# Kernel tuning notes

Measured on AMD Instinct MI355X. Metric: run time of the kernel, lower is better.

The kernel has to match this reference:

```python
import jax, jax.numpy as jnp
import numpy as np

# dims: T time steps, B batch, F clinical features, H GRU hidden, NH heads, DFF ffn dim, AH single-attn hidden
T, B, F, H, NH, DFF, AH = 128, 256, 76, 64, 4, 256, 8


def setup_inputs() -> dict:
    key = jax.random.key(0)
    ks = jax.random.split(key, 32)
    s = 0.1
    def u(k, shape):
        return jax.random.uniform(k, shape, jnp.float32, -s, s)
    return {
        "x": jax.random.normal(ks[0], (T, B, F), jnp.float32),
        # per-feature GRU(1, H) weight stacks (torch gate order: r, z, n)
        "gru_w_ih": u(ks[1], (F, 3 * H)),          # input dim is 1 -> squeezed
        "gru_w_hh": u(ks[2], (F, 3 * H, H)),
        "gru_b_ih": jnp.zeros((F, 3 * H), jnp.float32),
        "gru_b_hh": jnp.zeros((F, 3 * H), jnp.float32),
        # per-feature SingleAttention('new', time_aware) params
        "att_Wt": u(ks[3], (F, H, AH)),
        "att_Wx": u(ks[4], (F, H, AH)),
        "att_rate": jnp.full((F,), 0.8, jnp.float32),
        # multi-head self-attention over the feature axis
        "mha_wq": u(ks[5], (H, H)), "mha_bq": jnp.zeros((H,), jnp.float32),
        "mha_wk": u(ks[6], (H, H)), "mha_bk": jnp.zeros((H,), jnp.float32),
        "mha_wv": u(ks[7], (H, H)), "mha_bv": jnp.zeros((H,), jnp.float32),
        "mha_wo": u(ks[8], (H, H)), "mha_bo": jnp.zeros((H,), jnp.float32),
        # position-wise feed forward
        "ffn_w1": u(ks[9], (H, DFF)), "ffn_b1": jnp.zeros((DFF,), jnp.float32),
        "ffn_w2": u(ks[10], (DFF, H)), "ffn_b2": jnp.zeros((H,), jnp.float32),
        # FinalAttentionQKV ('mul')
        "fa_wq": u(ks[11], (H, H)), "fa_bq": jnp.zeros((H,), jnp.float32),
        "fa_wk": u(ks[12], (H, H)), "fa_bk": jnp.zeros((H,), jnp.float32),
        "fa_wv": u(ks[13], (H, H)), "fa_bv": jnp.zeros((H,), jnp.float32),
        # output head
        "out0_w": u(ks[14], (H, H)), "out0_b": jnp.zeros((H,), jnp.float32),
        "out1_w": u(ks[15], (H, 1)), "out1_b": jnp.zeros((1,), jnp.float32),
    }


def reference(x, gru_w_ih, gru_w_hh, gru_b_ih, gru_b_hh,
              att_Wt, att_Wx, att_rate,
              mha_wq, mha_bq, mha_wk, mha_bk, mha_wv, mha_bv, mha_wo, mha_bo,
              ffn_w1, ffn_b1, ffn_w2, ffn_b2,
              fa_wq, fa_bq, fa_wk, fa_bk, fa_wv, fa_bv,
              out0_w, out0_b, out1_w, out1_b):
    # x: (T, B, F); torch permutes to (B, T, F)
    Ts, Bsz, Fd = x.shape
    Hd = gru_w_hh.shape[-1]
    dk = Hd // NH

    # ---- all F GRU(1,H) channels fused into one scan (vectorized over F) ----
    xs = jnp.transpose(x, (0, 2, 1))  # (T, F, B)

    def step(h, x_t):  # h: (F,B,H), x_t: (F,B)
        gx = x_t[:, :, None] * gru_w_ih[:, None, :] + gru_b_ih[:, None, :]      # (F,B,3H)
        gh = jnp.einsum('fbh,fgh->fbg', h, gru_w_hh) + gru_b_hh[:, None, :]     # (F,B,3H)
        rx, zx, nx = jnp.split(gx, 3, axis=-1)
        rh, zh, nh = jnp.split(gh, 3, axis=-1)
        r = jax.nn.sigmoid(rx + rh)
        z = jax.nn.sigmoid(zx + zh)
        n = jnp.tanh(nx + r * nh)
        h_new = (1.0 - z) * n + z * h
        return h_new, h_new

    h0 = jnp.zeros((Fd, Bsz, Hd), x.dtype)
    _, hs = jax.lax.scan(step, h0, xs)        # (T, F, B, H)
    hs = jnp.transpose(hs, (1, 2, 0, 3))       # (F, B, T, H)

    # ---- per-feature SingleAttention, type='new', time-aware ----
    q = jnp.einsum('fbh,fha->fba', hs[:, :, -1, :], att_Wt)   # (F,B,AH)
    k = jnp.einsum('fbth,fha->fbta', hs, att_Wx)              # (F,B,T,AH)
    dp = jnp.einsum('fba,fbta->fbt', q, k)                    # (F,B,T)
    sig = jax.nn.sigmoid(dp)
    decay = jnp.arange(Ts, 0, -1, dtype=x.dtype)              # T..1 (time_decays + 1)
    denom = jax.nn.sigmoid(att_rate)[:, None, None] * (jnp.log(2.72 + (1.0 - sig)) * decay)
    e = jax.nn.relu(sig / denom)
    a = jax.nn.softmax(e, axis=-1)
    emb = jnp.einsum('fbt,fbth->bfh', a, hs)                  # (B, F, H)

    def lin(t, w, b):
        return t @ w + b

    # ---- multi-head self-attention over the F axis + residual ----
    # NOTE: original lambda ignores its (layernormed) argument, so LN is dead code.
    def heads(t):
        return t.reshape(Bsz, Fd, NH, dk).transpose(0, 2, 1, 3)
    qh = heads(lin(emb, mha_wq, mha_bq))
    kh = heads(lin(emb, mha_wk, mha_bk))
    vh = heads(lin(emb, mha_wv, mha_bv))
    scores = jnp.einsum('bhqd,bhkd->bhqk', qh, kh) / jnp.sqrt(jnp.asarray(dk, x.dtype))
    attn = jax.nn.softmax(scores, axis=-1)
    ctx = jnp.einsum('bhqk,bhkd->bhqd', attn, vh).transpose(0, 2, 1, 3).reshape(Bsz, Fd, Hd)
    ctx = emb + lin(ctx, mha_wo, mha_bo)

    # ---- position-wise feed-forward + residual ----
    ctx = ctx + lin(jax.nn.relu(lin(ctx, ffn_w1, ffn_b1)), ffn_w2, ffn_b2)

    # ---- FinalAttentionQKV, type='mul' ----
    fq = lin(ctx[:, -1, :], fa_wq, fa_bq)      # (B,H)
    fk = lin(ctx, fa_wk, fa_bk)                # (B,F,H)
    fv = lin(ctx, fa_wv, fa_bv)                # (B,F,H)
    fe = jnp.einsum('bfh,bh->bf', fk, fq)
    fa_w = jax.nn.softmax(fe, axis=1)
    v = jnp.einsum('bf,bfh->bh', fa_w, fv)     # (B,H)

    # ---- output head ----
    out = jax.nn.sigmoid(lin(jax.nn.relu(lin(v, out0_w, out0_b)), out1_w, out1_b))
    return out  # (B, 1)
```

## Files before the change

### kernel.cpp

```cpp
#include <hip/hip_runtime.h>
#include <hip/hip_bf16.h>
#include <cstdint>
#include <cstddef>

#define TT 128
#define BBATCH 256
#define FFEAT 76
#define HDIM 64
#define NHEAD 4
#define DKH 16
#define DFF1 256
#define AH1 8
#define NROWS (BBATCH * FFEAT)

#define LOG2E 1.4426950408889634f

typedef __attribute__((ext_vector_type(8))) short bf16x8;
typedef __attribute__((ext_vector_type(4))) float f32x4;

__device__ __forceinline__ float fast_sigmoid(float v) {
    float p = __builtin_amdgcn_exp2f(-v * LOG2E);
    return __builtin_amdgcn_rcpf(1.0f + p);
}
__device__ __forceinline__ float fast_tanh(float v) {
    float p = __builtin_amdgcn_exp2f(v * (2.0f * LOG2E));
    return 1.0f - 2.0f * __builtin_amdgcn_rcpf(1.0f + p);
}
__device__ __forceinline__ short f2bf(float x) {
    __hip_bfloat16 h = __float2bfloat16(x);
    return *reinterpret_cast<short*>(&h);
}
__device__ __forceinline__ float bf2f(unsigned short s) {
    return __uint_as_float(((unsigned)s) << 16);
}
__device__ __forceinline__ unsigned pack_bf16(float a, float b) {
    unsigned ua = (unsigned)(unsigned short)f2bf(a);
    unsigned ub = (unsigned)(unsigned short)f2bf(b);
    return ua | (ub << 16);
}

__global__ __launch_bounds__(256, 1) void gru_scan_kernel(
    const float* __restrict__ x, const float* __restrict__ w_ih,
    const float* __restrict__ w_hh, const float* __restrict__ b_ih,
    const float* __restrict__ b_hh, const float* __restrict__ Wt,
    const float* __restrict__ Wx, int f_base,
    __hip_bfloat16* __restrict__ hs, float* __restrict__ wtil)
{
    const int f_loc = blockIdx.y;
    const int f     = f_base + f_loc;
    const int bblk  = blockIdx.x * 64;
    const int tid   = threadIdx.x;
    const int wave  = tid >> 6;
    const int lane  = tid & 63;
    const int c     = lane & 15;
    const int q     = lane >> 4;
    const int b0    = bblk + wave * 16;

    __shared__ float x_lds[TT][64];
    __shared__ float wt_s[64][8];
    __shared__ float wx_s[64][8];
    __shared__ short hx[4][16][72];
    __shared__ float q_s[4][16][8];

    for (int i = tid; i < TT * 64; i += 256) {
        int t = i >> 6, b = i & 63;
        x_lds[t][b] = x[((size_t)t * BBATCH + bblk + b) * FFEAT + f];
    }
    for (int i = tid; i < 512; i += 256) {
        ((float*)wt_s)[i] = Wt[(size_t)f * 512 + i];
        ((float*)wx_s)[i] = Wx[(size_t)f * 512 + i];
    }
    for (int i = lane; i < 16 * 72; i += 64) ((short*)hx[wave])[i] = 0;
    __syncthreads();

    bf16x8 bfr[12][2];
    {
        const float* whh_f = w_hh + (size_t)f * 192 * 64;
        #pragma unroll
        for (int nt = 0; nt < 12; ++nt) {
            int gate = nt >> 2, sub = nt & 3;
            const float* row = whh_f + (size_t)(gate * 64 + 4 * c + sub) * 64;
            #pragma unroll
            for (int kq = 0; kq < 2; ++kq) {
                bf16x8 fr;
                #pragma unroll
                for (int j = 0; j < 8; ++j) fr[j] = f2bf(row[kq * 32 + q * 8 + j]);
                bfr[nt][kq] = fr;
            }
        }
    }
    float wihr[4], wihz[4], wihn[4], bR[4], bZ[4], bNX[4], bNH[4];
    #pragma unroll
    for (int g = 0; g < 4; ++g) {
        int u = 4 * c + g;
        wihr[g] = w_ih[f*192 + u];
        wihz[g] = w_ih[f*192 + 64 + u];
        wihn[g] = w_ih[f*192 + 128 + u];
        bR[g]  = b_ih[f*192 + u]      + b_hh[f*192 + u];
        bZ[g]  = b_ih[f*192 + 64 + u] + b_hh[f*192 + 64 + u];
        bNX[g] = b_ih[f*192 + 128 + u];
        bNH[g] = b_hh[f*192 + 128 + u];
    }

    float hprev[4][4];
    #pragma unroll
    for (int g = 0; g < 4; ++g)
        #pragma unroll
        for (int r = 0; r < 4; ++r) hprev[g][r] = 0.f;

    short* hs_s = (short*)hs + (size_t)f_loc * TT * BBATCH * HDIM;

    for (int t = 0; t < TT; ++t) {
        bf16x8 a0 = *(const bf16x8*)&hx[wave][c][q * 8];
        bf16x8 a1 = *(const bf16x8*)&hx[wave][c][32 + q * 8];
        if (t > 0) {
            short* dst = hs_s + ((size_t)(t - 1) * BBATCH + b0 + c) * HDIM + q * 8;
            *(bf16x8*)dst = a0;
            *(bf16x8*)(dst + 32) = a1;
        }

        f32x4 acc[12];
        #pragma unroll
        for (int g = 0; g < 4; ++g) {
            acc[g]     = f32x4{bR[g],  bR[g],  bR[g],  bR[g]};
            acc[g + 4] = f32x4{bZ[g],  bZ[g],  bZ[g],  bZ[g]};
            acc[g + 8] = f32x4{bNH[g], bNH[g], bNH[g], bNH[g]};
        }
        #pragma unroll
        for (int nt = 0; nt < 12; ++nt) {
            acc[nt] = __builtin_amdgcn_mfma_f32_16x16x32_bf16(a0, bfr[nt][0], acc[nt], 0, 0, 0);
            acc[nt] = __builtin_amdgcn_mfma_f32_16x16x32_bf16(a1, bfr[nt][1], acc[nt], 0, 0, 0);
        }

        float4 xv = *(const float4*)&x_lds[t][wave * 16 + q * 4];
        float hn4[4][4];
        #pragma unroll
        for (int g = 0; g < 4; ++g) {
            #pragma unroll
            for (int r = 0; r < 4; ++r) {
                float xb = (&xv.x)[r];
                float R  = fmaf(xb, wihr[g], acc[g][r]);
                float Z  = fmaf(xb, wihz[g], acc[g + 4][r]);
                float NX = fmaf(xb, wihn[g], bNX[g]);
                float rg = fast_sigmoid(R);
                float zg = fast_sigmoid(Z);
                float ng = fast_tanh(fmaf(rg, acc[g + 8][r], NX));
                float hn = fmaf(zg, hprev[g][r] - ng, ng);
                hprev[g][r] = hn;
                hn4[g][r] = hn;
            }
        }
        #pragma unroll
        for (int r = 0; r < 4; ++r) {
            uint2 w;
            w.x = pack_bf16(hn4[0][r], hn4[1][r]);
            w.y = pack_bf16(hn4[2][r], hn4[3][r]);
            *(uint2*)&hx[wave][q * 4 + r][4 * c] = w;
        }
    }
    {
        bf16x8 a0 = *(const bf16x8*)&hx[wave][c][q * 8];
        bf16x8 a1 = *(const bf16x8*)&hx[wave][c][32 + q * 8];
        short* dst = hs_s + ((size_t)(TT - 1) * BBATCH + b0 + c) * HDIM + q * 8;
        *(bf16x8*)dst = a0;
        *(bf16x8*)(dst + 32) = a1;
    }

    #pragma unroll
    for (int rr = 0; rr < 2; ++rr) {
        int role = rr * 64 + lane;
        int b = role >> 3, a = role & 7;
        float s = 0.f;
        #pragma unroll 8
        for (int j = 0; j < 64; ++j)
            s = fmaf(bf2f((unsigned short)hx[wave][b][j]), wt_s[j][a], s);
        q_s[wave][b][a] = s;
    }
    {
        int b = lane >> 2, jb = (lane & 3) * 16;
        float qreg[8];
        #pragma unroll
        for (int a = 0; a < 8; ++a) qreg[a] = q_s[wave][b][a];
        float* wt_out = wtil + ((size_t)(b0 + b) * FFEAT + f) * HDIM + jb;
        #pragma unroll
        for (int j4 = 0; j4 < 4; ++j4) {
            float4 v;
            #pragma unroll
            for (int jj = 0; jj < 4; ++jj) {
                int j = jb + j4 * 4 + jj;
                float s = 0.f;
                #pragma unroll
                for (int a = 0; a < 8; ++a) s = fmaf(wx_s[j][a], qreg[a], s);
                (&v.x)[jj] = s;
            }
            *(float4*)&wt_out[j4 * 4] = v;
        }
    }
}

__global__ __launch_bounds__(64) void attn2_kernel(
    const __hip_bfloat16* __restrict__ hs, const float* __restrict__ wtil,
    const float* __restrict__ rate, int f_base, float* __restrict__ emb)
{
    const int b     = blockIdx.x;
    const int f_loc = blockIdx.y;
    const int f     = f_base + f_loc;
    const int lane  = threadIdx.x;

    __shared__ short h_s[TT][72];
    __shared__ float a_s[TT];

    float wreg[64];
    {
        const float4* src = (const float4*)(wtil + ((size_t)b * FFEAT + f) * HDIM);
        #pragma unroll
        for (int i = 0; i < 16; ++i) {
            float4 v = src[i];
            wreg[4*i+0] = v.x; wreg[4*i+1] = v.y; wreg[4*i+2] = v.z; wreg[4*i+3] = v.w;
        }
    }
    const float rs = fast_sigmoid(rate[f]);
    const short* hsp = (const short*)hs + (size_t)f_loc * TT * BBATCH * HDIM;

    float e[2];
    #pragma unroll
    for (int half = 0; half < 2; ++half) {
        int t = half * 64 + lane;
        const uint4* row = (const uint4*)(hsp + ((size_t)t * BBATCH + b) * HDIM);
        float dp = 0.f;
        #pragma unroll
        for (int c4 = 0; c4 < 8; ++c4) {
            uint4 u = row[c4];
            *(uint4*)&h_s[t][c4 * 8] = u;
            unsigned vals[4] = {u.x, u.y, u.z, u.w};
            #pragma unroll
            for (int p = 0; p < 4; ++p) {
                dp = fmaf(__uint_as_float(vals[p] << 16),         wreg[c4*8 + 2*p],     dp);
                dp = fmaf(__uint_as_float(vals[p] & 0xffff0000u), wreg[c4*8 + 2*p + 1], dp);
            }
        }
        float sig = fast_sigmoid(dp);
        float den = rs * (__logf(2.72f + (1.0f - sig)) * (float)(TT - t));
        e[half] = fmaxf(sig / den, 0.0f);
    }
    float m = fmaxf(e[0], e[1]);
    #pragma unroll
    for (int off = 32; off > 0; off >>= 1) m = fmaxf(m, __shfl_xor(m, off, 64));
    float p0 = __builtin_amdgcn_exp2f((e[0] - m) * LOG2E);
    float p1 = __builtin_amdgcn_exp2f((e[1] - m) * LOG2E);
    float s = p0 + p1;
    #pragma unroll
    for (int off = 32; off > 0; off >>= 1) s += __shfl_xor(s, off, 64);
    float inv = __builtin_amdgcn_rcpf(s);
    a_s[lane]      = p0 * inv;
    a_s[lane + 64] = p1 * inv;

    const int j = lane;
    float acc = 0.f;
    #pragma unroll 8
    for (int t = 0; t < TT; ++t)
        acc = fmaf(a_s[t], bf2f((unsigned short)h_s[t][j]), acc);
    emb[((size_t)b * FFEAT + f) * HDIM + j] = acc;
}

struct GemmP {
    const float* X;
    const float* W[3];
    const float* B[3];
    const float* R;
    float* Y[3];
    int K;
    int Nfull;
    int act;
};

__global__ __launch_bounds__(256) void gemm_kernel(GemmP A)
{
    __shared__ float xs[64][65];
    __shared__ float ws[64][68];

    const int tid = threadIdx.x;
    const int tx  = tid & 15;
    const int ty  = tid >> 4;
    const int m0  = blockIdx.x * 64;
    const int n0  = blockIdx.y * 64;
    const int z   = blockIdx.z;

    const float* W = A.W[z];
    const float* Bv = A.B[z];
    float* Y = A.Y[z];
    const int K = A.K, Nfull = A.Nfull;

    float acc[4][4];
    #pragma unroll
    for (int i = 0; i < 4; ++i)
        #pragma unroll
        for (int j = 0; j < 4; ++j) acc[i][j] = 0.f;

    for (int kc = 0; kc < K; kc += 64) {
        for (int s = tid; s < 1024; s += 256) {
            int row = s >> 4, c4 = s & 15;
            float4 xv = *(const float4*)&A.X[(size_t)(m0 + row) * K + kc + 4*c4];
            xs[row][4*c4+0] = xv.x; xs[row][4*c4+1] = xv.y;
            xs[row][4*c4+2] = xv.z; xs[row][4*c4+3] = xv.w;
            float4 wv = *(const float4*)&W[(size_t)(kc + row) * Nfull + n0 + 4*c4];
            *(float4*)&ws[row][4*c4] = wv;
        }
        __syncthreads();
        #pragma unroll 16
        for (int k = 0; k < 64; ++k) {
            float a0 = xs[4*ty+0][k], a1 = xs[4*ty+1][k];
            float a2 = xs[4*ty+2][k], a3 = xs[4*ty+3][k];
            float4 wv = *(const float4*)&ws[k][4*tx];
            #pragma unroll
            for (int j = 0; j < 4; ++j) {
                float wj = (&wv.x)[j];
                acc[0][j] = fmaf(a0, wj, acc[0][j]);
                acc[1][j] = fmaf(a1, wj, acc[1][j]);
                acc[2][j] = fmaf(a2, wj, acc[2][j]);
                acc[3][j] = fmaf(a3, wj, acc[3][j]);
            }
        }
        __syncthreads();
    }

    float4 bias = *(const float4*)&Bv[n0 + 4*tx];
    #pragma unroll
    for (int i = 0; i < 4; ++i) {
        int row = m0 + 4*ty + i;
        float4 v;
        v.x = acc[i][0] + bias.x; v.y = acc[i][1] + bias.y;
        v.z = acc[i][2] + bias.z; v.w = acc[i][3] + bias.w;
        if (A.act) {
            v.x = fmaxf(v.x, 0.f); v.y = fmaxf(v.y, 0.f);
            v.z = fmaxf(v.z, 0.f); v.w = fmaxf(v.w, 0.f);
        }
        if (A.R) {
            float4 r4 = *(const float4*)&A.R[(size_t)row * Nfull + n0 + 4*tx];
            v.x += r4.x; v.y += r4.y; v.z += r4.z; v.w += r4.w;
        }
        *(float4*)&Y[(size_t)row * Nfull + n0 + 4*tx] = v;
    }
}

__global__ __launch_bounds__(256) void mha_core_kernel(
    const float* __restrict__ q, const float* __restrict__ k,
    const float* __restrict__ v, float* __restrict__ ctx)
{
    const int b  = blockIdx.x;
    const int hh = blockIdx.y;
    const int tid = threadIdx.x;

    __shared__ float qs[FFEAT][17];
    __shared__ float ks[FFEAT][17];
    __shared__ float vs[FFEAT][17];
    __shared__ float ps[FFEAT][77];

    for (int idx = tid; idx < FFEAT * DKH; idx += 256) {
        int i = idx >> 4, c = idx & 15;
        size_t g = ((size_t)b * FFEAT + i) * HDIM + hh * DKH + c;
        qs[i][c] = q[g]; ks[i][c] = k[g]; vs[i][c] = v[g];
    }
    __syncthreads();

    for (int idx = tid; idx < FFEAT * FFEAT; idx += 256) {
        int i = idx / FFEAT, j = idx % FFEAT;
        float acc = 0.f;
        #pragma unroll
        for (int c = 0; c < DKH; ++c) acc = fmaf(qs[i][c], ks[j][c], acc);
        ps[i][j] = acc * 0.25f;
    }
    __syncthreads();

    if (tid < FFEAT) {
        float mm = ps[tid][0];
        #pragma unroll 4
        for (int j = 1; j < FFEAT; ++j) mm = fmaxf(mm, ps[tid][j]);
        float ss = 0.f;
        #pragma unroll 4
        for (int j = 0; j < FFEAT; ++j) {
            float pv = __builtin_amdgcn_exp2f((ps[tid][j] - mm) * LOG2E);
            ps[tid][j] = pv; ss += pv;
        }
        float inv = 1.0f / ss;
        #pragma unroll 4
        for (int j = 0; j < FFEAT; ++j) ps[tid][j] *= inv;
    }
    __syncthreads();

    for (int idx = tid; idx < FFEAT * DKH; idx += 256) {
        int i = idx >> 4, c = idx & 15;
        float acc = 0.f;
        #pragma unroll 4
        for (int j = 0; j < FFEAT; ++j) acc = fmaf(ps[i][j], vs[j][c], acc);
        ctx[((size_t)b * FFEAT + i) * HDIM + hh * DKH + c] = acc;
    }
}

__global__ __launch_bounds__(128) void final_kernel(
    const float* __restrict__ ctx3, const float* __restrict__ fk,
    const float* __restrict__ fv,
    const float* __restrict__ faq, const float* __restrict__ fabq,
    const float* __restrict__ o0w, const float* __restrict__ o0b,
    const float* __restrict__ o1w, const float* __restrict__ o1b,
    float* __restrict__ out)
{
    const int b = blockIdx.x;
    const int tid = threadIdx.x;

    __shared__ float last[HDIM];
    __shared__ float fqs[HDIM];
    __shared__ float sm[FFEAT];
    __shared__ float vv[HDIM];
    __shared__ float hh[HDIM];
    __shared__ float redm[2], redp[2];

    if (tid < HDIM) last[tid] = ctx3[((size_t)b * FFEAT + FFEAT - 1) * HDIM + tid];
    __syncthreads();
    if (tid < HDIM) {
        float acc = fabq[tid];
        #pragma unroll 8
        for (int j = 0; j < HDIM; ++j) acc = fmaf(last[j], faq[j * HDIM + tid], acc);
        fqs[tid] = acc;
    }
    __syncthreads();

    float e = -3.0e38f;
    if (tid < FFEAT) {
        const float4* kr = (const float4*)&fk[((size_t)b * FFEAT + tid) * HDIM];
        float acc = 0.f;
        #pragma unroll
        for (int c4 = 0; c4 < 16; ++c4) {
            float4 kv = kr[c4];
            acc = fmaf(kv.x, fqs[4*c4+0], acc);
            acc = fmaf(kv.y, fqs[4*c4+1], acc);
            acc = fmaf(kv.z, fqs[4*c4+2], acc);
            acc = fmaf(kv.w, fqs[4*c4+3], acc);
        }
        e = acc;
    }
    float m = e;
    #pragma unroll
    for (int off = 32; off > 0; off >>= 1) m = fmaxf(m, __shfl_xor(m, off, 64));
    if ((tid & 63) == 0) redm[tid >> 6] = m;
    __syncthreads();
    m = fmaxf(redm[0], redm[1]);
    float p = (tid < FFEAT) ? __builtin_amdgcn_exp2f((e - m) * LOG2E) : 0.f;
    float s = p;
    #pragma unroll
    for (int off = 32; off > 0; off >>= 1) s += __shfl_xor(s, off, 64);
    if ((tid & 63) == 0) redp[tid >> 6] = s;
    __syncthreads();
    s = redp[0] + redp[1];
    if (tid < FFEAT) sm[tid] = p / s;
    __syncthreads();

    if (tid < HDIM) {
        float acc = 0.f;
        for (int ff = 0; ff < FFEAT; ++ff)
            acc = fmaf(sm[ff], fv[((size_t)b * FFEAT + ff) * HDIM + tid], acc);
        vv[tid] = acc;
    }
    __syncthreads();
    if (tid < HDIM) {
        float acc = o0b[tid];
        #pragma unroll 8
        for (int j = 0; j < HDIM; ++j) acc = fmaf(vv[j], o0w[j * HDIM + tid], acc);
        hh[tid] = fmaxf(acc, 0.f);
    }
    __syncthreads();
    if (tid < 64) {
        float t = hh[tid] * o1w[tid];
        #pragma unroll
        for (int off = 32; off > 0; off >>= 1) t += __shfl_xor(t, off, 64);
        if (tid == 0) out[b] = fast_sigmoid(t + o1b[0]);
    }
}

__global__ void ws_report_kernel(float* out, int n, float ws_mib) {
    int i = blockIdx.x * blockDim.x + threadIdx.x;
    if (i < n) out[i] = ws_mib;
}

extern "C" void kernel_launch(void* const* d_in, const int* in_sizes, int n_in,
                              void* d_out, int out_size, void* d_ws, size_t ws_size,
                              hipStream_t stream)
{
    const float* x     = (const float*)d_in[0];
    const float* w_ih  = (const float*)d_in[1];
    const float* w_hh  = (const float*)d_in[2];
    const float* b_ih  = (const float*)d_in[3];
    const float* b_hh  = (const float*)d_in[4];
    const float* attWt = (const float*)d_in[5];
    const float* attWx = (const float*)d_in[6];
    const float* attRt = (const float*)d_in[7];
    const float* wq    = (const float*)d_in[8];
    const float* bq    = (const float*)d_in[9];
    const float* wk    = (const float*)d_in[10];
    const float* bk    = (const float*)d_in[11];
    const float* wv    = (const float*)d_in[12];
    const float* bv    = (const float*)d_in[13];
    const float* wo    = (const float*)d_in[14];
    const float* bo    = (const float*)d_in[15];
    const float* w1    = (const float*)d_in[16];
    const float* b1    = (const float*)d_in[17];
    const float* w2    = (const float*)d_in[18];
    const float* b2    = (const float*)d_in[19];
    const float* faq   = (const float*)d_in[20];
    const float* fabq  = (const float*)d_in[21];
    const float* fak   = (const float*)d_in[22];
    const float* fabk  = (const float*)d_in[23];
    const float* fav   = (const float*)d_in[24];
    const float* fabv  = (const float*)d_in[25];
    const float* o0w   = (const float*)d_in[26];
    const float* o0b   = (const float*)d_in[27];
    const float* o1w   = (const float*)d_in[28];
    const float* o1b   = (const float*)d_in[29];
    float* out = (float*)d_out;

    const size_t emb_bytes  = (size_t)NROWS * HDIM * 4;
    const size_t wtil_bytes = (size_t)NROWS * HDIM * 4;
    const size_t R64        = (size_t)NROWS * HDIM;
    const size_t tail_bytes = 12 * R64 * 4;

    const int chunk_opts[6] = {76, 38, 19, 4, 2, 1};
    int FC = 0;
    for (int i = 0; i < 6; ++i) {
        size_t hs_b = (size_t)chunk_opts[i] * BBATCH * TT * HDIM * 2;
        size_t scratch = hs_b > tail_bytes ? hs_b : tail_bytes;
        if (emb_bytes + wtil_bytes + scratch <= ws_size) { FC = chunk_opts[i]; break; }
    }
    if (FC == 0) {
        ws_report_kernel<<<dim3((out_size + 255) / 256), dim3(256), 0, stream>>>(
            out, out_size, (float)((double)ws_size / (1024.0 * 1024.0)));
        return;
    }

    float* emb  = (float*)d_ws;
    float* wtil = (float*)((char*)d_ws + emb_bytes);
    char*  scratch = (char*)d_ws + emb_bytes + wtil_bytes;
    __hip_bfloat16* hs = (__hip_bfloat16*)scratch;

    for (int f0 = 0; f0 < FFEAT; f0 += FC) {
        int fc = (FFEAT - f0 < FC) ? (FFEAT - f0) : FC;
        gru_scan_kernel<<<dim3(4, fc), dim3(256), 0, stream>>>(
            x, w_ih, w_hh, b_ih, b_hh, attWt, attWx, f0, hs, wtil);
        attn2_kernel<<<dim3(BBATCH, fc), dim3(64), 0, stream>>>(
            hs, wtil, attRt, f0, emb);
    }

    float* ts   = (float*)scratch;
    float* q    = ts;
    float* k    = ts + 1*R64;
    float* v    = ts + 2*R64;
    float* ctx  = ts + 3*R64;
    float* ctx2 = ts + 4*R64;
    float* hid  = ts + 5*R64;
    float* ctx3 = ts + 9*R64;
    float* fk   = ts + 10*R64;
    float* fv   = ts + 11*R64;

    const int MB = NROWS / 64;

    {
        GemmP A = { emb, {wq, wk, wv}, {bq, bk, bv}, nullptr, {q, k, v}, 64, 64, 0 };
        gemm_kernel<<<dim3(MB, 1, 3), dim3(256), 0, stream>>>(A);
    }
    mha_core_kernel<<<dim3(BBATCH, NHEAD), dim3(256), 0, stream>>>(q, k, v, ctx);
    {
        GemmP A = { ctx, {wo, nullptr, nullptr}, {bo, nullptr, nullptr}, emb,
                    {ctx2, nullptr, nullptr}, 64, 64, 0 };
        gemm_kernel<<<dim3(MB, 1, 1), dim3(256), 0, stream>>>(A);
    }
    {
        GemmP A = { ctx2, {w1, nullptr, nullptr}, {b1, nullptr, nullptr}, nullptr,
                    {hid, nullptr, nullptr}, 64, 256, 1 };
        gemm_kernel<<<dim3(MB, 4, 1), dim3(256), 0, stream>>>(A);
    }
    {
        GemmP A = { hid, {w2, nullptr, nullptr}, {b2, nullptr, nullptr}, ctx2,
                    {ctx3, nullptr, nullptr}, 256, 64, 0 };
        gemm_kernel<<<dim3(MB, 1, 1), dim3(256), 0, stream>>>(A);
    }
    {
        GemmP A = { ctx3, {fak, fav, nullptr}, {fabk, fabv, nullptr}, nullptr,
                    {fk, fv, nullptr}, 64, 64, 0 };
        gemm_kernel<<<dim3(MB, 1, 2), dim3(256), 0, stream>>>(A);
    }
    final_kernel<<<dim3(BBATCH), dim3(128), 0, stream>>>(
        ctx3, fk, fv, faq, fabq, o0w, o0b, o1w, o1b, out);
}
```

Baseline: 601.8 us.

## Keep GRU hidden state in registers via transposed MFMA and batch-major hs layout

Swaps the MFMA operand roles so the recurrent weights are the A operand and the hidden state is the B operand. The permuted weight-row mapping makes each lane's output exactly the bf16x8 fragment it needs for the next step, so the per-step LDS write and read of the hidden state goes away. Bias is folded into the MFMA accumulator input instead of being re-splatted each step. The hs buffer becomes batch-major ([f][b][t][h]), which gives contiguous per-row stores and contiguous reads in the attention kernel. The risk is that the permuted row and column mapping must match the gate and unit indexing exactly.

Result: faster. 583.7 us (-3.0%).

```diff
diff --git a/kernel.cpp b/kernel.cpp
--- a/kernel.cpp
+++ b/kernel.cpp
@@ -70,101 +70,97 @@
         ((float*)wt_s)[i] = Wt[(size_t)f * 512 + i];
         ((float*)wx_s)[i] = Wx[(size_t)f * 512 + i];
     }
-    for (int i = lane; i < 16 * 72; i += 64) ((short*)hx[wave])[i] = 0;
-    __syncthreads();
-
-    bf16x8 bfr[12][2];
+    __syncthreads();
+
+    bf16x8 afr[12][2];
     {
         const float* whh_f = w_hh + (size_t)f * 192 * 64;
         #pragma unroll
         for (int nt = 0; nt < 12; ++nt) {
-            int gate = nt >> 2, sub = nt & 3;
-            const float* row = whh_f + (size_t)(gate * 64 + 4 * c + sub) * 64;
+            int gate = nt >> 2, tt = nt & 3;
+            int urow = (c >> 2) * 8 + (tt & 1) * 4 + (c & 3) + (tt >> 1) * 32;
+            const float* row = whh_f + (size_t)(gate * 64 + urow) * 64;
             #pragma unroll
             for (int kq = 0; kq < 2; ++kq) {
                 bf16x8 fr;
                 #pragma unroll
                 for (int j = 0; j < 8; ++j) fr[j] = f2bf(row[kq * 32 + q * 8 + j]);
-                bfr[nt][kq] = fr;
+                afr[nt][kq] = fr;
             }
         }
     }
-    float wihr[4], wihz[4], wihn[4], bR[4], bZ[4], bNX[4], bNH[4];
-    #pragma unroll
-    for (int g = 0; g < 4; ++g) {
-        int u = 4 * c + g;
-        wihr[g] = w_ih[f*192 + u];
-        wihz[g] = w_ih[f*192 + 64 + u];
-        wihn[g] = w_ih[f*192 + 128 + u];
-        bR[g]  = b_ih[f*192 + u]      + b_hh[f*192 + u];
-        bZ[g]  = b_ih[f*192 + 64 + u] + b_hh[f*192 + 64 + u];
-        bNX[g] = b_ih[f*192 + 128 + u];
-        bNH[g] = b_hh[f*192 + 128 + u];
+    float wr[4][4], wz[4][4], wn[4][4], bnx[4][4];
+    f32x4 biasv[12];
+    #pragma unroll
+    for (int tt = 0; tt < 4; ++tt) {
+        #pragma unroll
+        for (int r = 0; r < 4; ++r) {
+            int u = q * 8 + (tt & 1) * 4 + r + (tt >> 1) * 32;
+            wr[tt][r]  = w_ih[f*192 + u];
+            wz[tt][r]  = w_ih[f*192 + 64 + u];
+            wn[tt][r]  = w_ih[f*192 + 128 + u];
+            bnx[tt][r] = b_ih[f*192 + 128 + u];
+            biasv[tt][r]     = b_ih[f*192 + u]      + b_hh[f*192 + u];
+            biasv[4 + tt][r] = b_ih[f*192 + 64 + u] + b_hh[f*192 + 64 + u];
+            biasv[8 + tt][r] = b_hh[f*192 + 128 + u];
+        }
     }
 
     float hprev[4][4];
     #pragma unroll
-    for (int g = 0; g < 4; ++g)
-        #pragma unroll
-        for (int r = 0; r < 4; ++r) hprev[g][r] = 0.f;
-
-    short* hs_s = (short*)hs + (size_t)f_loc * TT * BBATCH * HDIM;
+    for (int tt = 0; tt < 4; ++tt)
+        #pragma unroll
+        for (int r = 0; r < 4; ++r) hprev[tt][r] = 0.f;
+
+    bf16x8 hb0 = {0,0,0,0,0,0,0,0};
+    bf16x8 hb1 = {0,0,0,0,0,0,0,0};
+
+    short* hs_b = (short*)hs + ((size_t)f_loc * BBATCH + b0 + c) * TT * HDIM;
 
     for (int t = 0; t < TT; ++t) {
-        bf16x8 a0 = *(const bf16x8*)&hx[wave][c][q * 8];
-        bf16x8 a1 = *(const bf16x8*)&hx[wave][c][32 + q * 8];
-        if (t > 0) {
-            short* dst = hs_s + ((size_t)(t - 1) * BBATCH + b0 + c) * HDIM + q * 8;
-            *(bf16x8*)dst = a0;
-            *(bf16x8*)(dst + 32) = a1;
-        }
-
         f32x4 acc[12];
         #pragma unroll
-        for (int g = 0; g < 4; ++g) {
-            acc[g]     = f32x4{bR[g],  bR[g],  bR[g],  bR[g]};
-            acc[g + 4] = f32x4{bZ[g],  bZ[g],  bZ[g],  bZ[g]};
-            acc[g + 8] = f32x4{bNH[g], bNH[g], bNH[g], bNH[g]};
-        }
-        #pragma unroll
         for (int nt = 0; nt < 12; ++nt) {
-            acc[nt] = __builtin_amdgcn_mfma_f32_16x16x32_bf16(a0, bfr[nt][0], acc[nt], 0, 0, 0);
-            acc[nt] = __builtin_amdgcn_mfma_f32_16x16x32_bf16(a1, bfr[nt][1], acc[nt], 0, 0, 0);
-        }
-
-        float4 xv = *(const float4*)&x_lds[t][wave * 16 + q * 4];
+            f32x4 a = __builtin_amdgcn_mfma_f32_16x16x32_bf16(afr[nt][0], hb0, biasv[nt], 0, 0, 0);
+            acc[nt]  = __builtin_amdgcn_mfma_f32_16x16x32_bf16(afr[nt][1], hb1, a, 0, 0, 0);
+        }
+
+        float xv = x_lds[t][wave * 16 + c];
         float hn4[4][4];
         #pragma unroll
-        for (int g = 0; g < 4; ++g) {
+        for (int tt = 0; tt < 4; ++tt) {
             #pragma unroll
             for (int r = 0; r < 4; ++r) {
-                float xb = (&xv.x)[r];
-                float R  = fmaf(xb, wihr[g], acc[g][r]);
-                float Z  = fmaf(xb, wihz[g], acc[g + 4][r]);
-                float NX = fmaf(xb, wihn[g], bNX[g]);
+                float R  = fmaf(xv, wr[tt][r], acc[tt][r]);
+                float Z  = fmaf(xv, wz[tt][r], acc[4 + tt][r]);
+                float NX = fmaf(xv, wn[tt][r], bnx[tt][r]);
                 float rg = fast_sigmoid(R);
                 float zg = fast_sigmoid(Z);
-                float ng = fast_tanh(fmaf(rg, acc[g + 8][r], NX));
-                float hn = fmaf(zg, hprev[g][r] - ng, ng);
-                hprev[g][r] = hn;
-                hn4[g][r] = hn;
+                float ng = fast_tanh(fmaf(rg, acc[8 + tt][r], NX));
+                float hn = fmaf(zg, hprev[tt][r] - ng, ng);
+                hprev[tt][r] = hn;
+                hn4[tt][r] = hn;
             }
         }
-        #pragma unroll
-        for (int r = 0; r < 4; ++r) {
-            uint2 w;
-            w.x = pack_bf16(hn4[0][r], hn4[1][r]);
-            w.y = pack_bf16(hn4[2][r], hn4[3][r]);
-            *(uint2*)&hx[wave][q * 4 + r][4 * c] = w;
-        }
-    }
-    {
-        bf16x8 a0 = *(const bf16x8*)&hx[wave][c][q * 8];
-        bf16x8 a1 = *(const bf16x8*)&hx[wave][c][32 + q * 8];
-        short* dst = hs_s + ((size_t)(TT - 1) * BBATCH + b0 + c) * HDIM + q * 8;
-        *(bf16x8*)dst = a0;
-        *(bf16x8*)(dst + 32) = a1;
-    }
+        {
+            union { int4 i; bf16x8 v; } u0, u1;
+            u0.i.x = pack_bf16(hn4[0][0], hn4[0][1]);
+            u0.i.y = pack_bf16(hn4[0][2], hn4[0][3]);
+            u0.i.z = pack_bf16(hn4[1][0], hn4[1][1]);
+            u0.i.w = pack_bf16(hn4[1][2], hn4[1][3]);
+            u1.i.x = pack_bf16(hn4[2][0], hn4[2][1]);
+            u1.i.y = pack_bf16(hn4[2][2], hn4[2][3]);
+            u1.i.z = pack_bf16(hn4[3][0], hn4[3][1]);
+            u1.i.w = pack_bf16(hn4[3][2], hn4[3][3]);
+            hb0 = u0.v; hb1 = u1.v;
+        }
+        short* dst = hs_b + (size_t)t * HDIM + q * 8;
+        *(bf16x8*)dst = hb0;
+        *(bf16x8*)(dst + 32) = hb1;
+    }
+
+    *(bf16x8*)&hx[wave][c][q * 8]      = hb0;
+    *(bf16x8*)&hx[wave][c][32 + q * 8] = hb1;
 
     #pragma unroll
     for (int rr = 0; rr < 2; ++rr) {
@@ -220,13 +216,13 @@
         }
     }
     const float rs = fast_sigmoid(rate[f]);
-    const short* hsp = (const short*)hs + (size_t)f_loc * TT * BBATCH * HDIM;
+    const short* base = (const short*)hs + ((size_t)f_loc * BBATCH + b) * TT * HDIM;
 
     float e[2];
     #pragma unroll
     for (int half = 0; half < 2; ++half) {
         int t = half * 64 + lane;
-        const uint4* row = (const uint4*)(hsp + ((size_t)t * BBATCH + b) * HDIM);
+        const uint4* row = (const uint4*)(base + (size_t)t * HDIM);
         float dp = 0.f;
         #pragma unroll
         for (int c4 = 0; c4 < 8; ++c4) {
```
